# Performance work log

Hardware: AMD Instinct MI355X
Metric: run time of the kernel (lower is better)

The kernel has to match this reference:

```python
import jax, jax.numpy as jnp
import numpy as np

T, B, D, H = 512, 128, 256, 256
SIGMA = 0.01


def setup_inputs() -> dict:
    key = jax.random.key(0)
    ks = jax.random.split(key, 5)
    inputs = jax.random.normal(ks[0], (T, B, D), dtype=jnp.float32)
    W_xh_f = jax.random.normal(ks[1], (D, H), dtype=jnp.float32) * SIGMA
    W_hh_f = jax.random.normal(ks[2], (H, H), dtype=jnp.float32) * SIGMA
    b_h_f = jnp.zeros((H,), dtype=jnp.float32)
    W_xh_b = jax.random.normal(ks[3], (D, H), dtype=jnp.float32) * SIGMA
    W_hh_b = jax.random.normal(ks[4], (H, H), dtype=jnp.float32) * SIGMA
    b_h_b = jnp.zeros((H,), dtype=jnp.float32)
    return {"inputs": inputs, "W_xh_f": W_xh_f, "W_hh_f": W_hh_f, "b_h_f": b_h_f,
            "W_xh_b": W_xh_b, "W_hh_b": W_hh_b, "b_h_b": b_h_b}


def _rnn(inputs, W_xh, W_hh, b_h):
    # inputs: [T, B, D]; returns outputs [T, B, H], final state [B, H]
    h0 = jnp.zeros((inputs.shape[1], W_hh.shape[0]), dtype=inputs.dtype)
    # Precompute input projections for all steps (one big GEMM).
    xW = jnp.einsum('tbd,dh->tbh', inputs, W_xh) + b_h

    def step(h, xw_t):
        h = jnp.tanh(xw_t + h @ W_hh)
        return h, h

    hT, outs = jax.lax.scan(step, h0, xW)
    return outs, hT


def reference(inputs, W_xh_f, W_hh_f, b_h_f, W_xh_b, W_hh_b, b_h_b):
    f_outs, f_H = _rnn(inputs, W_xh_f, W_hh_f, b_h_f)          # forward direction
    b_outs, b_H = _rnn(inputs[::-1], W_xh_b, W_hh_b, b_h_b)    # backward direction
    # align backward outputs with original time order and concat on feature dim
    outputs = jnp.concatenate([f_outs, b_outs[::-1]], axis=-1)  # [T, B, 2H]
    return outputs, f_H, b_H
```

## Files before the change

kernel.cpp:

```cpp
#include <hip/hip_runtime.h>
#include <hip/hip_bf16.h>
#include <stdint.h>


typedef short sh8   __attribute__((ext_vector_type(8)));
typedef float f32x4 __attribute__((ext_vector_type(4)));

#define TT 512
#define BB 128
#define HH 256
#define LDH 264

__device__ __forceinline__ unsigned short f2bf(float x) {
    union { float f; unsigned u; } v; v.f = x;
    unsigned r = v.u + 0x7FFFu + ((v.u >> 16) & 1u);
    return (unsigned short)(r >> 16);
}
__device__ __forceinline__ unsigned pk2bf(float lo, float hi) {
    union { __hip_bfloat162 b; unsigned u; } c;
    c.b = __float22bfloat162_rn(make_float2(lo, hi));
    return c.u;
}
__device__ __forceinline__ float tanh5(float x) {
    float e = __builtin_amdgcn_exp2f(x * 2.8853900817779268f);
    return __builtin_fmaf(-2.0f, __builtin_amdgcn_rcpf(e + 1.0f), 1.0f);
}
__device__ __forceinline__ void bar_lds() {
    asm volatile("s_waitcnt lgkmcnt(0)\n\ts_barrier" ::: "memory");
}
__device__ __forceinline__ sh8 pack8(float4 a, float4 b) {
    union { sh8 s; unsigned u[4]; } c;
    c.u[0] = pk2bf(a.x, a.y); c.u[1] = pk2bf(a.z, a.w);
    c.u[2] = pk2bf(b.x, b.y); c.u[3] = pk2bf(b.z, b.w);
    return c.s;
}

__global__ __launch_bounds__(512, 2) void xw_precompute(
    const float* __restrict__ x,
    const float* __restrict__ Wxf, const float* __restrict__ bhf,
    const float* __restrict__ Wxb, const float* __restrict__ bhb,
    float* __restrict__ out)
{
    __shared__ __align__(16) unsigned short xb[2][16 * LDH];

    const int tid = threadIdx.x;
    const int w  = tid >> 6, l = tid & 63;
    const int li = l & 15, lq = l >> 4;
    const int N0 = w * 32;
    const int dir = blockIdx.x >> 8;
    const int r0  = (blockIdx.x & 255) * 256;
    const float* W  = dir ? Wxb : Wxf;
    const float* bs = dir ? bhb : bhf;

    sh8 wf[2][8];
#pragma unroll
    for (int nt = 0; nt < 2; ++nt)
#pragma unroll
        for (int kf = 0; kf < 8; ++kf) {
            sh8 t;
#pragma unroll
            for (int j = 0; j < 8; ++j)
                t[j] = (short)f2bf(W[(size_t)(kf * 32 + lq * 8 + j) * HH + N0 + nt * 16 + li]);
            wf[nt][kf] = t;
        }
    f32x4 bias4[2];
#pragma unroll
    for (int nt = 0; nt < 2; ++nt)
        bias4[nt] = *(const f32x4*)&bs[N0 + nt * 16 + lq * 4];

    const int sm = tid >> 5;
    const int sk = (tid & 31) * 8;
    const float* xrow = x + (size_t)(r0 + sm) * HH + sk;

    {
        float4 v0 = *(const float4*)xrow;
        float4 v1 = *(const float4*)(xrow + 4);
        *(sh8*)&xb[0][sm * LDH + sk] = pack8(v0, v1);
    }
    float4 xg0 = *(const float4*)(xrow + 16 * HH);
    float4 xg1 = *(const float4*)(xrow + 16 * HH + 4);
    bar_lds();

    float* obase = out + (size_t)(r0 + li) * 512 + dir * HH + N0 + lq * 4;

    for (int t = 0; t < 16; ++t) {
        const int cur = t & 1, nxt = cur ^ 1;
        {
            *(sh8*)&xb[nxt][sm * LDH + sk] = pack8(xg0, xg1);
            const int t2 = (t + 2 < 16) ? t + 2 : t;
            const float* p = xrow + (size_t)t2 * (16 * HH);
            xg0 = *(const float4*)p;
            xg1 = *(const float4*)(p + 4);
        }
        sh8 xf[8];
#pragma unroll
        for (int kf = 0; kf < 8; ++kf)
            xf[kf] = *(const sh8*)&xb[cur][li * LDH + kf * 32 + lq * 8];

        f32x4 acc[2];
#pragma unroll
        for (int nt = 0; nt < 2; ++nt)
            acc[nt] = __builtin_amdgcn_mfma_f32_16x16x32_bf16(
                wf[nt][0], xf[0], bias4[nt], 0, 0, 0);
#pragma unroll
        for (int kf = 1; kf < 8; ++kf)
#pragma unroll
            for (int nt = 0; nt < 2; ++nt)
                acc[nt] = __builtin_amdgcn_mfma_f32_16x16x32_bf16(
                    wf[nt][kf], xf[kf], acc[nt], 0, 0, 0);

        float* op = obase + (size_t)t * (16 * 512);
#pragma unroll
        for (int nt = 0; nt < 2; ++nt)
            *(f32x4*)(op + nt * 16) = acc[nt];
        bar_lds();
    }
}

__global__ __launch_bounds__(512, 2) void rnn_recur(
    const float* __restrict__ Whf, const float* __restrict__ Whb,
    float* __restrict__ out)
{
    __shared__ __align__(16) unsigned short hb[2][16 * LDH];

    const int tid = threadIdx.x;
    const int w  = tid >> 6, l = tid & 63;
    const int li = l & 15, lq = l >> 4;
    const int dir   = blockIdx.x >> 3;
    const int bbase = (blockIdx.x & 7) * 16;
    const float* Wh = dir ? Whb : Whf;
    const int N0 = w * 32;

    sh8 wfh[2][8];
#pragma unroll
    for (int nt = 0; nt < 2; ++nt)
#pragma unroll
        for (int kf = 0; kf < 8; ++kf) {
            sh8 t;
#pragma unroll
            for (int j = 0; j < 8; ++j)
                t[j] = (short)f2bf(Wh[(size_t)(kf * 32 + lq * 8 + j) * HH + N0 + nt * 16 + li]);
            wfh[nt][kf] = t;
        }

    for (int i = tid; i < 16 * LDH / 2; i += 512) ((unsigned*)hb[0])[i] = 0u;

    const ptrdiff_t ostep = dir ? -(ptrdiff_t)(BB * 512) : (ptrdiff_t)(BB * 512);
    const int t0 = dir ? TT - 1 : 0;
    float* op = out + (size_t)t0 * (BB * 512)
                    + (size_t)(bbase + li) * 512 + dir * HH + N0 + lq * 4;
    const float* pf = op + 4 * ostep;
    float* fsp = out + (size_t)TT * BB * 512 + (size_t)dir * (BB * HH)
                     + (size_t)(bbase + li) * HH + N0 + lq * 4;

    f32x4 xA[2], xB[2], xC[2], xD[2];
#pragma unroll
    for (int nt = 0; nt < 2; ++nt) {
        xA[nt] = *(const f32x4*)(op + 0 * ostep + nt * 16);
        xB[nt] = *(const f32x4*)(op + 1 * ostep + nt * 16);
        xC[nt] = *(const f32x4*)(op + 2 * ostep + nt * 16);
        xD[nt] = *(const f32x4*)(op + 3 * ostep + nt * 16);
    }

    const unsigned short* hr0 = &hb[0][li * LDH + lq * 8];
    const unsigned short* hr1 = &hb[1][li * LDH + lq * 8];
    unsigned short*       hw0 = &hb[0][li * LDH + N0 + lq * 4];
    unsigned short*       hw1 = &hb[1][li * LDH + N0 + lq * 4];

    bar_lds();

#define STEP(s_, HR, HW, XU)                                                    \
    do {                                                                        \
        sh8 hf[8];                                                              \
        _Pragma("unroll")                                                       \
        for (int kf = 0; kf < 8; ++kf)                                          \
            hf[kf] = *(const sh8*)(HR + kf * 32);                               \
        f32x4 acc[2];                                                           \
        __builtin_amdgcn_s_setprio(1);                                          \
        _Pragma("unroll")                                                       \
        for (int nt = 0; nt < 2; ++nt)        \
            acc[nt] = __builtin_amdgcn_mfma_f32_16x16x32_bf16(                  \
                wfh[nt][0], hf[0], XU[nt], 0, 0, 0);                            \
        _Pragma("unroll")                                                       \
        for (int nt = 0; nt < 2; ++nt)              \
            XU[nt] = *(const f32x4*)(pf + nt * 16);                             \
        pf += ((s_) + 5 < TT) ? ostep : 0;           \
        _Pragma("unroll")                                                       \
        for (int kf = 1; kf < 8; ++kf)                                          \
            _Pragma("unroll")                                                   \
            for (int nt = 0; nt < 2; ++nt)                                      \
                acc[nt] = __builtin_amdgcn_mfma_f32_16x16x32_bf16(              \
                    wfh[nt][kf], hf[kf], acc[nt], 0, 0, 0);                     \
        __builtin_amdgcn_s_setprio(0);                                          \
        f32x4 vv[2];                                                            \
        _Pragma("unroll")                                                       \
        for (int nt = 0; nt < 2; ++nt) {                                        \
            f32x4 v;                                                            \
            v[0] = tanh5(acc[nt][0]);                                           \
            v[1] = tanh5(acc[nt][1]);                                           \
            v[2] = tanh5(acc[nt][2]);                                           \
            v[3] = tanh5(acc[nt][3]);                                           \
            vv[nt] = v;                                                         \
            *(f32x4*)(op + nt * 16) = v;            \
            unsigned plo = pk2bf(v[0], v[1]);                                   \
            unsigned phi = pk2bf(v[2], v[3]);                                   \
            *(uint2*)(HW + nt * 16) = make_uint2(plo, phi);                     \
        }                                                                       \
        if ((s_) == TT - 1) {                                                   \
            _Pragma("unroll")                                                   \
            for (int nt = 0; nt < 2; ++nt)                                      \
                *(f32x4*)(fsp + nt * 16) = vv[nt];                              \
        }                                                                       \
        op += ostep;                                                            \
        bar_lds();                                                              \
    } while (0)

    for (int s = 0; s < TT; s += 4) {
        STEP(s,     hr0, hw1, xA);
        STEP(s + 1, hr1, hw0, xB);
        STEP(s + 2, hr0, hw1, xC);
        STEP(s + 3, hr1, hw0, xD);
    }
#undef STEP
}

extern "C" void kernel_launch(void* const* d_in, const int* in_sizes, int n_in,
                              void* d_out, int out_size, void* d_ws, size_t ws_size,
                              hipStream_t stream)
{
    const float* x   = (const float*)d_in[0];
    const float* Wxf = (const float*)d_in[1];
    const float* Whf = (const float*)d_in[2];
    const float* bhf = (const float*)d_in[3];
    const float* Wxb = (const float*)d_in[4];
    const float* Whb = (const float*)d_in[5];
    const float* bhb = (const float*)d_in[6];

    hipLaunchKernelGGL(xw_precompute, dim3(512), dim3(512), 0, stream,
                       x, Wxf, bhf, Wxb, bhb, (float*)d_out);
    hipLaunchKernelGGL(rnn_recur, dim3(16), dim3(512), 0, stream,
                       Whf, Whb, (float*)d_out);
}
```

Measured before the change: 635.7 us.

## Drop LDS staging in input projection; load x directly into MFMA fragments

The input-projection kernel now uses 256-thread blocks where each wave covers 64 output columns instead of 32. Each lane loads its x fragment straight from global memory into registers and converts it to bf16 there, which removes the shared-memory staging buffer and the per-step barriers. A two-buffer register ping-pong prefetches the next timestep's fragments while the current one runs its MFMAs. The cost is higher register pressure (twice the weight fragments, two x buffers) and redundant global reads of x across the four waves, which the cache must absorb. The recurrent kernel, which likely dominates total time, is unchanged.

```diff
diff --git a/kernel.cpp b/kernel.cpp
--- a/kernel.cpp
+++ b/kernel.cpp
@@ -35,26 +35,24 @@
     return c.s;
 }
 
-__global__ __launch_bounds__(512, 2) void xw_precompute(
+__global__ __launch_bounds__(256, 2) void xw_precompute(
     const float* __restrict__ x,
     const float* __restrict__ Wxf, const float* __restrict__ bhf,
     const float* __restrict__ Wxb, const float* __restrict__ bhb,
     float* __restrict__ out)
 {
-    __shared__ __align__(16) unsigned short xb[2][16 * LDH];
-
     const int tid = threadIdx.x;
     const int w  = tid >> 6, l = tid & 63;
     const int li = l & 15, lq = l >> 4;
-    const int N0 = w * 32;
-    const int dir = blockIdx.x >> 8;
-    const int r0  = (blockIdx.x & 255) * 256;
+    const int dir = blockIdx.x & 1;
+    const int r0  = (blockIdx.x >> 1) * 256;
     const float* W  = dir ? Wxb : Wxf;
     const float* bs = dir ? bhb : bhf;
-
-    sh8 wf[2][8];
-#pragma unroll
-    for (int nt = 0; nt < 2; ++nt)
+    const int N0 = w * 64;
+
+    sh8 wf[4][8];
+#pragma unroll
+    for (int nt = 0; nt < 4; ++nt)
 #pragma unroll
         for (int kf = 0; kf < 8; ++kf) {
             sh8 t;
@@ -63,58 +61,55 @@
                 t[j] = (short)f2bf(W[(size_t)(kf * 32 + lq * 8 + j) * HH + N0 + nt * 16 + li]);
             wf[nt][kf] = t;
         }
-    f32x4 bias4[2];
-#pragma unroll
-    for (int nt = 0; nt < 2; ++nt)
+    f32x4 bias4[4];
+#pragma unroll
+    for (int nt = 0; nt < 4; ++nt)
         bias4[nt] = *(const f32x4*)&bs[N0 + nt * 16 + lq * 4];
 
-    const int sm = tid >> 5;
-    const int sk = (tid & 31) * 8;
-    const float* xrow = x + (size_t)(r0 + sm) * HH + sk;
-
-    {
-        float4 v0 = *(const float4*)xrow;
-        float4 v1 = *(const float4*)(xrow + 4);
-        *(sh8*)&xb[0][sm * LDH + sk] = pack8(v0, v1);
+    const float* xr = x + (size_t)(r0 + li) * HH + lq * 8;
+    float* ob = out + (size_t)(r0 + li) * 512 + dir * HH + N0 + lq * 4;
+
+#define LOADT(t_, XF)                                                           \
+    do {                                                                        \
+        const float* p_ = xr + (size_t)(t_) * (16 * HH);                        \
+        _Pragma("unroll")                                                       \
+        for (int kf = 0; kf < 8; ++kf) {                                        \
+            float4 a_ = *(const float4*)(p_ + kf * 32);                         \
+            float4 b_ = *(const float4*)(p_ + kf * 32 + 4);                     \
+            XF[kf] = pack8(a_, b_);                                             \
+        }                                                                       \
+    } while (0)
+
+#define COMPT(t_, XF)                                                           \
+    do {                                                                        \
+        f32x4 acc[4];                                                           \
+        _Pragma("unroll")                                                       \
+        for (int nt = 0; nt < 4; ++nt)                      \
+            acc[nt] = __builtin_amdgcn_mfma_f32_16x16x32_bf16(                  \
+                wf[nt][0], XF[0], bias4[nt], 0, 0, 0);                          \
+        _Pragma("unroll")                                                       \
+        for (int kf = 1; kf < 8; ++kf)                                          \
+            _Pragma("unroll")                                                   \
+            for (int nt = 0; nt < 4; ++nt)                                      \
+                acc[nt] = __builtin_amdgcn_mfma_f32_16x16x32_bf16(              \
+                    wf[nt][kf], XF[kf], acc[nt], 0, 0, 0);                      \
+        float* op_ = ob + (size_t)(t_) * (16 * 512);                            \
+        _Pragma("unroll")                                                       \
+        for (int nt = 0; nt < 4; ++nt)                                          \
+            *(f32x4*)(op_ + nt * 16) = acc[nt];                                 \
+    } while (0)
+
+    sh8 xfA[8], xfB[8];
+    LOADT(0, xfA);
+#pragma unroll
+    for (int t = 0; t < 16; t += 2) {
+        if (t + 1 < 16) LOADT(t + 1, xfB);
+        COMPT(t, xfA);
+        if (t + 2 < 16) LOADT(t + 2, xfA);
+        COMPT(t + 1, xfB);
     }
-    float4 xg0 = *(const float4*)(xrow + 16 * HH);
-    float4 xg1 = *(const float4*)(xrow + 16 * HH + 4);
-    bar_lds();
-
-    float* obase = out + (size_t)(r0 + li) * 512 + dir * HH + N0 + lq * 4;
-
-    for (int t = 0; t < 16; ++t) {
-        const int cur = t & 1, nxt = cur ^ 1;
-        {
-            *(sh8*)&xb[nxt][sm * LDH + sk] = pack8(xg0, xg1);
-            const int t2 = (t + 2 < 16) ? t + 2 : t;
-            const float* p = xrow + (size_t)t2 * (16 * HH);
-            xg0 = *(const float4*)p;
-            xg1 = *(const float4*)(p + 4);
-        }
-        sh8 xf[8];
-#pragma unroll
-        for (int kf = 0; kf < 8; ++kf)
-            xf[kf] = *(const sh8*)&xb[cur][li * LDH + kf * 32 + lq * 8];
-
-        f32x4 acc[2];
-#pragma unroll
-        for (int nt = 0; nt < 2; ++nt)
-            acc[nt] = __builtin_amdgcn_mfma_f32_16x16x32_bf16(
-                wf[nt][0], xf[0], bias4[nt], 0, 0, 0);
-#pragma unroll
-        for (int kf = 1; kf < 8; ++kf)
-#pragma unroll
-            for (int nt = 0; nt < 2; ++nt)
-                acc[nt] = __builtin_amdgcn_mfma_f32_16x16x32_bf16(
-                    wf[nt][kf], xf[kf], acc[nt], 0, 0, 0);
-
-        float* op = obase + (size_t)t * (16 * 512);
-#pragma unroll
-        for (int nt = 0; nt < 2; ++nt)
-            *(f32x4*)(op + nt * 16) = acc[nt];
-        bar_lds();
-    }
+#undef LOADT
+#undef COMPT
 }
 
 __global__ __launch_bounds__(512, 2) void rnn_recur(
@@ -236,7 +231,7 @@
     const float* Whb = (const float*)d_in[5];
     const float* bhb = (const float*)d_in[6];
 
-    hipLaunchKernelGGL(xw_precompute, dim3(512), dim3(512), 0, stream,
+    hipLaunchKernelGGL(xw_precompute, dim3(512), dim3(256), 0, stream,
                        x, Wxf, bhf, Wxb, bhb, (float*)d_out);
     hipLaunchKernelGGL(rnn_recur, dim3(16), dim3(512), 0, stream,
                        Whf, Whb, (float*)d_out);
```

After: 752.2 us. 1.18x slower.
